# Performance work log

Measured on AMD Instinct MI355X. Metric: run time of the kernel, lower is better.

Reference implementation:

```python
import jax, jax.numpy as jnp
import numpy as np

EPS = 1e-6


def setup_inputs() -> dict:
    key = jax.random.key(0)
    k1, k2 = jax.random.split(key)
    B, Lq, Lk, D = 16, 1024, 1024, 512
    query = jax.random.normal(k1, (B, Lq, D), dtype=jnp.float32)
    context = jax.random.normal(k2, (B, Lk, D), dtype=jnp.float32)
    gamma = jnp.ones((D,), dtype=jnp.float32)
    beta = jnp.zeros((D,), dtype=jnp.float32)
    return {"query": query, "context": context, "gamma": gamma, "beta": beta}


def _layer_norm(x, gamma, beta):
    mean = jnp.mean(x, axis=-1, keepdims=True)
    var = jnp.var(x, axis=-1, keepdims=True)
    return gamma * (x - mean) * jax.lax.rsqrt(var + EPS) + beta


def reference(query, context, gamma, beta):
    # query: [B, Lq, D], context: [B, Lk, D]
    D = query.shape[-1]
    scale = 1.0 / np.sqrt(D).astype(np.float32)
    # additive-style tanh-activated scores: [B, Lq, Lk]
    score = jnp.tanh(jnp.einsum('bqd,bkd->bqk', query, context) * scale)
    attn = jax.nn.softmax(score, axis=2)
    # dropout is identity in eval/reference mode
    out = jnp.einsum('bqk,bkd->bqd', attn, context)
    out = _layer_norm(out + query, gamma, beta)
    return out
```

## Files before the change

kernel.cpp:

```cpp
#include <hip/hip_runtime.h>
#include <hip/hip_bf16.h>
#include <cstdint>

#define LQ 1024
#define LK 1024
#define DD 512
#define NB 16
#define QB 64
#define KB 32
#define NT (LK / KB)
#define CSTRIDE 1088
#define CSZ (32 * CSTRIDE)

typedef short bf16x8 __attribute__((ext_vector_type(8)));
typedef float f32x4 __attribute__((ext_vector_type(4)));

__device__ __forceinline__ uint16_t f2bf(float f) {
  uint32_t u = __builtin_bit_cast(uint32_t, f);
  u = (u + 0x7fffu + ((u >> 16) & 1u)) >> 16;
  return (uint16_t)u;
}

__device__ __forceinline__ void load_lds16(const void* g, void* l) {
  __builtin_amdgcn_global_load_lds(
      (const __attribute__((address_space(1))) uint32_t*)g,
      (__attribute__((address_space(3))) uint32_t*)l, 16, 0, 0);
}

__global__ __launch_bounds__(256) void prep_kernel(const float* __restrict__ c,
                                                   uint16_t* __restrict__ cb,
                                                   uint16_t* __restrict__ ct) {
  __shared__ float t[32][33];
  const int k0 = blockIdx.x * 32, d0 = blockIdx.y * 32, b = blockIdx.z;
  const float* src = c + (size_t)b * LK * DD;
  uint16_t* cbd = cb + (size_t)b * LK * DD;
  uint16_t* ctd = ct + (size_t)b * DD * LK;
  const int tx = threadIdx.x, ty = threadIdx.y;
  for (int j = 0; j < 4; ++j) {
    int k = ty + j * 8;
    float v = src[(size_t)(k0 + k) * DD + d0 + tx];
    t[k][tx] = v;
    cbd[(size_t)(k0 + k) * DD + d0 + tx] = f2bf(v);
  }
  __syncthreads();
  for (int j = 0; j < 4; ++j) {
    int d = ty + j * 8;
    ctd[(size_t)(d0 + d) * LK + k0 + tx] = f2bf(t[tx][d]);
  }
}

__global__ __launch_bounds__(512, 2) void attn_kernel(
    const uint16_t* __restrict__ Cb, const uint16_t* __restrict__ Ctb,
    const float* __restrict__ Qf, const float* __restrict__ gamma,
    const float* __restrict__ beta, float* __restrict__ out) {
  __shared__ uint4 cs4[2 * CSZ / 16];
  __shared__ uint4 cts4[2 * 32 * 1024 / 16];
  __shared__ char plds[64 * 80];
  __shared__ float denom_s[QB];
  __shared__ float rsum_s[QB], rsumsq_s[QB], mean_s[QB], rstd_s[QB];

  const int tid = threadIdx.x;
  const int w = tid >> 6, l = tid & 63, c = l & 15, g = l >> 4;
  const int orig = blockIdx.x;
  const int virt = ((orig & 7) << 5) | (orig >> 3);
  const int b = virt >> 4, qblk = virt & 15;
  const int q0 = qblk * QB;
  const int mt = w & 1, qt = w >> 1;
  const float scale = 0.044194173824159216f;

  if (tid < QB) { denom_s[tid] = 0.f; rsum_s[tid] = 0.f; rsumsq_s[tid] = 0.f; }

  bf16x8 qfrag[16];
  {
    const float* qrow = Qf + ((size_t)b * LQ + q0 + qt * 16 + c) * DD;
    for (int s = 0; s < 16; ++s) {
      float4 a0 = *(const float4*)(qrow + s * 32 + g * 8);
      float4 a1 = *(const float4*)(qrow + s * 32 + g * 8 + 4);
      ushort4 u0, u1;
      u0.x = f2bf(a0.x); u0.y = f2bf(a0.y); u0.z = f2bf(a0.z); u0.w = f2bf(a0.w);
      u1.x = f2bf(a1.x); u1.y = f2bf(a1.y); u1.z = f2bf(a1.z); u1.w = f2bf(a1.w);
      union { ushort4 u[2]; bf16x8 v; } pk;
      pk.u[0] = u0; pk.u[1] = u1;
      qfrag[s] = pk.v;
    }
  }

  const int kkA = mt * 16 + c;
  const int aoff = kkA * CSTRIDE + ((g ^ (kkA & 3)) * 16);

  f32x4 oacc[4][4];
  for (int i = 0; i < 4; ++i)
    for (int j = 0; j < 4; ++j) oacc[i][j] = (f32x4){0.f, 0.f, 0.f, 0.f};
  float dacc = 0.f;

  const char* cbyte = (const char*)Cb + (size_t)b * LK * DD * 2;
  const char* ctbyte = (const char*)Ctb + (size_t)b * DD * LK * 2;

  int csrcoff[4];
  for (int j = 0; j < 4; ++j) {
    int r = w * 4 + j;
    csrcoff[j] = r * 1024 + ((l * 16) ^ ((r & 3) << 4));
  }

  char* cs0 = (char*)cs4;
  char* cs1 = cs0 + CSZ;
  char* cts0 = (char*)cts4;
  char* cts1 = cts0 + 32 * 1024;
  const int pwoff = (qt * 16 + c) * 80 + (mt * 16 + g * 4) * 2;
  const int proff = c * 80 + g * 16;

  auto stageC = [&](char* dst, int kt2) {
    const char* s0 = cbyte + (size_t)kt2 * 32768;
    for (int j = 0; j < 4; ++j)
      load_lds16(s0 + csrcoff[j], dst + (w * 4 + j) * CSTRIDE);
  };
  auto stageCT = [&](char* dst, int kt2) {
    const int kk0 = kt2 * KB;
    for (int j = 0; j < 4; ++j) {
      int d0l = w * 64 + j * 16;
      int d = d0l + (l >> 2);
      const char* src =
          ctbyte + (size_t)d * 2048 + kk0 * 2 + (((l & 3) * 16) ^ ((d & 3) << 4));
      load_lds16(src, dst + d0l * 64);
    }
  };

  stageC(cs0, 0);
  stageCT(cts0, 0);
  __syncthreads();

  for (int kt = 0; kt < NT; ++kt) {
    const int cur = kt & 1;
    const char* csR = cur ? cs1 : cs0;
    const char* ctsR = cur ? cts1 : cts0;
    if (kt + 1 < NT) {
      stageC(cur ? cs0 : cs1, kt + 1);
      stageCT(cur ? cts0 : cts1, kt + 1);
    }
    f32x4 s0v = {0.f, 0.f, 0.f, 0.f}, s1v = {0.f, 0.f, 0.f, 0.f};
    f32x4 s2v = {0.f, 0.f, 0.f, 0.f}, s3v = {0.f, 0.f, 0.f, 0.f};
    {
      const char* ar = csR + aoff;
      for (int s = 0; s < 4; ++s) {
        bf16x8 a0 = *(const bf16x8*)(ar + s * 64);
        bf16x8 a1 = *(const bf16x8*)(ar + (s + 4) * 64);
        bf16x8 a2 = *(const bf16x8*)(ar + (s + 8) * 64);
        bf16x8 a3 = *(const bf16x8*)(ar + (s + 12) * 64);
        s0v = __builtin_amdgcn_mfma_f32_16x16x32_bf16(a0, qfrag[s], s0v, 0, 0, 0);
        s1v = __builtin_amdgcn_mfma_f32_16x16x32_bf16(a1, qfrag[s + 4], s1v, 0, 0, 0);
        s2v = __builtin_amdgcn_mfma_f32_16x16x32_bf16(a2, qfrag[s + 8], s2v, 0, 0, 0);
        s3v = __builtin_amdgcn_mfma_f32_16x16x32_bf16(a3, qfrag[s + 12], s3v, 0, 0, 0);
      }
    }
    {
      float pv[4];
      for (int i = 0; i < 4; ++i) {
        float sv = ((s0v[i] + s1v[i]) + (s2v[i] + s3v[i])) * scale;
        float e2 = __expf(sv * 2.f);
        float r = __builtin_amdgcn_rcpf(e2 + 1.f);
        float th = (e2 - 1.f) * r;
        float p = __expf(th);
        pv[i] = p;
        dacc += p;
      }
      uint2 pk;
      pk.x = ((uint32_t)f2bf(pv[1]) << 16) | f2bf(pv[0]);
      pk.y = ((uint32_t)f2bf(pv[3]) << 16) | f2bf(pv[2]);
      *(uint2*)(plds + pwoff) = pk;
    }
    asm volatile("s_waitcnt lgkmcnt(0)" ::: "memory");
    __builtin_amdgcn_s_barrier();
    __builtin_amdgcn_sched_barrier(0);

    {
      bf16x8 pa[4], pb[4];
      for (int q2 = 0; q2 < 4; ++q2)
        pa[q2] = *(const bf16x8*)(plds + proff + q2 * 1280);
      for (int nt = 0; nt < 4; ++nt) {
        int d = w * 64 + nt * 16 + c;
        pb[nt] = *(const bf16x8*)(ctsR + d * 64 + ((g * 16) ^ ((d & 3) << 4)));
      }
      for (int q2 = 0; q2 < 4; ++q2)
        for (int n2 = 0; n2 < 4; ++n2)
          oacc[q2][n2] =
              __builtin_amdgcn_mfma_f32_16x16x32_bf16(pa[q2], pb[n2], oacc[q2][n2], 0, 0, 0);
    }
    __syncthreads();
  }

  float dv = dacc;
  dv += __shfl_xor(dv, 16);
  dv += __shfl_xor(dv, 32);
  if (l < 16) atomicAdd(&denom_s[qt * 16 + l], dv);
  __syncthreads();

  const float* qsrc = Qf + ((size_t)b * LQ + q0) * DD;
  for (int q2 = 0; q2 < 4; ++q2)
    for (int i = 0; i < 4; ++i) {
      int row = q2 * 16 + g * 4 + i;
      float inv = 1.f / denom_s[row];
      for (int nt = 0; nt < 4; ++nt) {
        int d = w * 64 + nt * 16 + c;
        float o = oacc[q2][nt][i] * inv + qsrc[(size_t)row * DD + d];
        oacc[q2][nt][i] = o;
      }
    }
  for (int q2 = 0; q2 < 4; ++q2)
    for (int i = 0; i < 4; ++i) {
      float s1 = 0.f, s2 = 0.f;
      for (int nt = 0; nt < 4; ++nt) {
        float v = oacc[q2][nt][i];
        s1 += v;
        s2 += v * v;
      }
      s1 += __shfl_xor(s1, 1); s2 += __shfl_xor(s2, 1);
      s1 += __shfl_xor(s1, 2); s2 += __shfl_xor(s2, 2);
      s1 += __shfl_xor(s1, 4); s2 += __shfl_xor(s2, 4);
      s1 += __shfl_xor(s1, 8); s2 += __shfl_xor(s2, 8);
      if (c == 0) {
        int row = q2 * 16 + g * 4 + i;
        atomicAdd(&rsum_s[row], s1);
        atomicAdd(&rsumsq_s[row], s2);
      }
    }
  __syncthreads();
  if (tid < QB) {
    float m = rsum_s[tid] * (1.f / DD);
    float var = rsumsq_s[tid] * (1.f / DD) - m * m;
    mean_s[tid] = m;
    rstd_s[tid] = rsqrtf(fmaxf(var, 0.f) + 1e-6f);
  }
  __syncthreads();
  float* op = out + ((size_t)b * LQ + q0) * DD;
  for (int q2 = 0; q2 < 4; ++q2)
    for (int i = 0; i < 4; ++i) {
      int row = q2 * 16 + g * 4 + i;
      float m = mean_s[row], r = rstd_s[row];
      for (int nt = 0; nt < 4; ++nt) {
        int d = w * 64 + nt * 16 + c;
        op[(size_t)row * DD + d] = gamma[d] * ((oacc[q2][nt][i] - m) * r) + beta[d];
      }
    }
}

__global__ __launch_bounds__(256) void naive_kernel(const float* __restrict__ Q,
                                                    const float* __restrict__ C,
                                                    const float* __restrict__ gamma,
                                                    const float* __restrict__ beta,
                                                    float* __restrict__ out) {
  const int row = blockIdx.x;
  const int b = row >> 10;
  const int tid = threadIdx.x;
  __shared__ float qs[DD];
  __shared__ float ps[LK];
  __shared__ float ys[DD];
  __shared__ float red[256];
  const float* qp = Q + (size_t)row * DD;
  const float* cb = C + (size_t)b * LK * DD;
  for (int d = tid; d < DD; d += 256) qs[d] = qp[d];
  __syncthreads();
  for (int k = tid; k < LK; k += 256) {
    const float* cr = cb + (size_t)k * DD;
    float s = 0.f;
    for (int d = 0; d < DD; ++d) s += qs[d] * cr[d];
    s *= 0.044194173824159216f;
    float e2 = __expf(2.f * s);
    float th = (e2 - 1.f) / (e2 + 1.f);
    ps[k] = __expf(th);
  }
  __syncthreads();
  float dsum = 0.f;
  for (int k = tid; k < LK; k += 256) dsum += ps[k];
  red[tid] = dsum;
  __syncthreads();
  for (int off = 128; off; off >>= 1) {
    if (tid < off) red[tid] += red[tid + off];
    __syncthreads();
  }
  float inv = 1.f / red[0];
  __syncthreads();
  for (int d = tid; d < DD; d += 256) {
    float o = 0.f;
    for (int k = 0; k < LK; ++k) o += ps[k] * cb[(size_t)k * DD + d];
    ys[d] = o * inv + qs[d];
  }
  __syncthreads();
  float s1 = 0.f;
  for (int d = tid; d < DD; d += 256) s1 += ys[d];
  red[tid] = s1;
  __syncthreads();
  for (int off = 128; off; off >>= 1) {
    if (tid < off) red[tid] += red[tid + off];
    __syncthreads();
  }
  float mean = red[0] * (1.f / DD);
  __syncthreads();
  float s2 = 0.f;
  for (int d = tid; d < DD; d += 256) {
    float v = ys[d] - mean;
    s2 += v * v;
  }
  red[tid] = s2;
  __syncthreads();
  for (int off = 128; off; off >>= 1) {
    if (tid < off) red[tid] += red[tid + off];
    __syncthreads();
  }
  float rstd = rsqrtf(red[0] * (1.f / DD) + 1e-6f);
  for (int d = tid; d < DD; d += 256)
    out[(size_t)row * DD + d] = gamma[d] * ((ys[d] - mean) * rstd) + beta[d];
}

extern "C" void kernel_launch(void* const* d_in, const int* in_sizes, int n_in,
                              void* d_out, int out_size, void* d_ws, size_t ws_size,
                              hipStream_t stream) {
  const float* Qf = (const float*)d_in[0];
  const float* Cf = (const float*)d_in[1];
  const float* gamma = (const float*)d_in[2];
  const float* beta = (const float*)d_in[3];
  float* out = (float*)d_out;
  const size_t nelem = (size_t)NB * LK * DD;
  const size_t need = nelem * 2 * 2;
  if (ws_size >= need) {
    uint16_t* Cb = (uint16_t*)d_ws;
    uint16_t* Ctb = Cb + nelem;
    prep_kernel<<<dim3(LK / 32, DD / 32, NB), dim3(32, 8), 0, stream>>>(Cf, Cb, Ctb);
    attn_kernel<<<256, 512, 0, stream>>>(Cb, Ctb, Qf, gamma, beta, out);
  } else {
    naive_kernel<<<NB * LQ, 256, 0, stream>>>(Qf, Cf, gamma, beta, out);
  }
}
```

Before: 83.24 us.

## Single-buffer C tiles with split-phase prefetch to fit four blocks per CU

Removes the double buffers for the C and C-transpose LDS tiles. Each half is now prefetched as soon as its consumer phase finishes: the next C tile is issued after the score barrier, and the next C-transpose tile after the PV MFMA barrier. This shrinks LDS use, and the launch bound is raised to 4 blocks per CU so more waves can hide latency. It also swaps manual bf16 rounding for the packed v_cvt_pk_bf16_f32 instruction. The trade-off is an extra barrier per iteration and a shorter prefetch window. The higher occupancy hint may also force register spills given the large oacc and qfrag arrays.

Result: slower. 243.9 us (+193.0%).

```diff
diff --git a/kernel.cpp b/kernel.cpp
--- a/kernel.cpp
+++ b/kernel.cpp
@@ -49,12 +49,12 @@
   }
 }
 
-__global__ __launch_bounds__(512, 2) void attn_kernel(
+__global__ __launch_bounds__(512, 4) void attn_kernel(
     const uint16_t* __restrict__ Cb, const uint16_t* __restrict__ Ctb,
     const float* __restrict__ Qf, const float* __restrict__ gamma,
     const float* __restrict__ beta, float* __restrict__ out) {
-  __shared__ uint4 cs4[2 * CSZ / 16];
-  __shared__ uint4 cts4[2 * 32 * 1024 / 16];
+  __shared__ uint4 cs4[CSZ / 16];
+  __shared__ uint4 cts4[32 * 1024 / 16];
   __shared__ char plds[64 * 80];
   __shared__ float denom_s[QB];
   __shared__ float rsum_s[QB], rsumsq_s[QB], mean_s[QB], rstd_s[QB];
@@ -102,45 +102,36 @@
     csrcoff[j] = r * 1024 + ((l * 16) ^ ((r & 3) << 4));
   }
 
-  char* cs0 = (char*)cs4;
-  char* cs1 = cs0 + CSZ;
-  char* cts0 = (char*)cts4;
-  char* cts1 = cts0 + 32 * 1024;
+  char* cs = (char*)cs4;
+  char* cts = (char*)cts4;
   const int pwoff = (qt * 16 + c) * 80 + (mt * 16 + g * 4) * 2;
   const int proff = c * 80 + g * 16;
 
-  auto stageC = [&](char* dst, int kt2) {
+  auto stageC = [&](int kt2) {
     const char* s0 = cbyte + (size_t)kt2 * 32768;
     for (int j = 0; j < 4; ++j)
-      load_lds16(s0 + csrcoff[j], dst + (w * 4 + j) * CSTRIDE);
+      load_lds16(s0 + csrcoff[j], cs + (w * 4 + j) * CSTRIDE);
   };
-  auto stageCT = [&](char* dst, int kt2) {
+  auto stageCT = [&](int kt2) {
     const int kk0 = kt2 * KB;
     for (int j = 0; j < 4; ++j) {
       int d0l = w * 64 + j * 16;
       int d = d0l + (l >> 2);
       const char* src =
           ctbyte + (size_t)d * 2048 + kk0 * 2 + (((l & 3) * 16) ^ ((d & 3) << 4));
-      load_lds16(src, dst + d0l * 64);
+      load_lds16(src, cts + d0l * 64);
     }
   };
 
-  stageC(cs0, 0);
-  stageCT(cts0, 0);
+  stageC(0);
+  stageCT(0);
   __syncthreads();
 
   for (int kt = 0; kt < NT; ++kt) {
-    const int cur = kt & 1;
-    const char* csR = cur ? cs1 : cs0;
-    const char* ctsR = cur ? cts1 : cts0;
-    if (kt + 1 < NT) {
-      stageC(cur ? cs0 : cs1, kt + 1);
-      stageCT(cur ? cts0 : cts1, kt + 1);
-    }
     f32x4 s0v = {0.f, 0.f, 0.f, 0.f}, s1v = {0.f, 0.f, 0.f, 0.f};
     f32x4 s2v = {0.f, 0.f, 0.f, 0.f}, s3v = {0.f, 0.f, 0.f, 0.f};
     {
-      const char* ar = csR + aoff;
+      const char* ar = cs + aoff;
       for (int s = 0; s < 4; ++s) {
         bf16x8 a0 = *(const bf16x8*)(ar + s * 64);
         bf16x8 a1 = *(const bf16x8*)(ar + (s + 4) * 64);
@@ -164,13 +155,14 @@
         dacc += p;
       }
       uint2 pk;
-      pk.x = ((uint32_t)f2bf(pv[1]) << 16) | f2bf(pv[0]);
-      pk.y = ((uint32_t)f2bf(pv[3]) << 16) | f2bf(pv[2]);
+      asm("v_cvt_pk_bf16_f32 %0, %1, %2" : "=v"(pk.x) : "v"(pv[0]), "v"(pv[1]));
+      asm("v_cvt_pk_bf16_f32 %0, %1, %2" : "=v"(pk.y) : "v"(pv[2]), "v"(pv[3]));
       *(uint2*)(plds + pwoff) = pk;
     }
     asm volatile("s_waitcnt lgkmcnt(0)" ::: "memory");
     __builtin_amdgcn_s_barrier();
     __builtin_amdgcn_sched_barrier(0);
+    if (kt + 1 < NT) stageC(kt + 1);
 
     {
       bf16x8 pa[4], pb[4];
@@ -178,13 +170,17 @@
         pa[q2] = *(const bf16x8*)(plds + proff + q2 * 1280);
       for (int nt = 0; nt < 4; ++nt) {
         int d = w * 64 + nt * 16 + c;
-        pb[nt] = *(const bf16x8*)(ctsR + d * 64 + ((g * 16) ^ ((d & 3) << 4)));
+        pb[nt] = *(const bf16x8*)(cts + d * 64 + ((g * 16) ^ ((d & 3) << 4)));
       }
       for (int q2 = 0; q2 < 4; ++q2)
         for (int n2 = 0; n2 < 4; ++n2)
           oacc[q2][n2] =
               __builtin_amdgcn_mfma_f32_16x16x32_bf16(pa[q2], pb[n2], oacc[q2][n2], 0, 0, 0);
     }
+    asm volatile("s_waitcnt lgkmcnt(0)" ::: "memory");
+    __builtin_amdgcn_s_barrier();
+    __builtin_amdgcn_sched_barrier(0);
+    if (kt + 1 < NT) stageCT(kt + 1);
     __syncthreads();
   }
 
```
